# Optimization experiments

Hardware: AMD Instinct MI355X
Metric: run time of the kernel (lower is better)

The kernel has to match this reference:

```python
import jax, jax.numpy as jnp
import numpy as np

B = 64          # number of jets
LVLS = 13       # tree levels (complete binary tree, 4096 leaves/jet)
F = 7           # input features
H = 64          # hidden size
SIZES = [B * (2 ** j) for j in range(LVLS)]
OFFS = np.concatenate([[0], np.cumsum(SIZES)])  # level offsets into flat contents


def setup_inputs() -> dict:
    key = jax.random.key(0)
    ks = jax.random.split(key, 9)
    n_total = int(OFFS[-1])  # 524224
    s = lambda k, shp, fan: jax.random.normal(k, shp, jnp.float32) / np.sqrt(fan)
    return {
        "contents": jax.random.normal(ks[0], (n_total, F), jnp.float32),
        "W_u": s(ks[1], (H, F), F),       "b_u": jnp.zeros((H,), jnp.float32),
        "W_r": s(ks[2], (3 * H, 3 * H), 3 * H), "b_r": jnp.zeros((3 * H,), jnp.float32),
        "W_h": s(ks[3], (H, 3 * H), 3 * H),     "b_h": jnp.zeros((H,), jnp.float32),
        "W_z": s(ks[4], (4 * H, 4 * H), 4 * H), "b_z": jnp.zeros((4 * H,), jnp.float32),
    }


def reference(contents, W_u, b_u, W_r, b_r, W_h, b_h, W_z, b_z):
    # Bottom-up recursive gated embedding (n_iters=0 path -> relu activation).
    up = None  # embedding of level j+1
    for j in reversed(range(LVLS)):
        c = contents[int(OFFS[j]):int(OFFS[j + 1])]        # [n_j, F]
        u = jax.nn.relu(c @ W_u.T + b_u)                   # [n_j, H]
        if j == LVLS - 1:
            up = u                                         # leaf level: no inners
            continue
        n = SIZES[j]
        # children of node k are (2k, 2k+1) at level j+1 -> strided gather
        h_L = up[0::2]                                     # [n_j, H]
        h_R = up[1::2]                                     # [n_j, H]
        hhu = jnp.concatenate([h_L, h_R, u], axis=1)       # [n_j, 3H]
        r = jax.nn.sigmoid(hhu @ W_r.T + b_r)              # reset gate
        h_H = jax.nn.relu((r * hhu) @ W_h.T + b_h)         # candidate
        z = jnp.concatenate([h_H, hhu], axis=1) @ W_z.T + b_z  # [n_j, 4H]
        g = jax.nn.softmax(z.reshape(n, 4, H), axis=1)     # softmax over 4 gates
        up = g[:, 0] * h_H + g[:, 1] * h_L + g[:, 2] * h_R + g[:, 3] * u
    return up.reshape(B, -1)                               # [B, H]
```

## Files before the change

kernel.cpp:

```cpp
#include <hip/hip_runtime.h>
#include <hip/hip_bf16.h>


#define LOG2E 1.4426950408889634f
#define OSTR 76

typedef __bf16 bf16x8 __attribute__((ext_vector_type(8)));
typedef unsigned short u16x8 __attribute__((ext_vector_type(8)));
typedef float f32x4 __attribute__((ext_vector_type(4)));
typedef unsigned short bfr;

__device__ __forceinline__ float bfr2f(bfr v) { return __uint_as_float(((unsigned)v) << 16); }
__device__ __forceinline__ bfr f2bfr(float f) {
    __hip_bfloat16 h = __float2bfloat16(f);
    return __builtin_bit_cast(bfr, h);
}
__device__ __forceinline__ float fexp2(float x) {
#if __has_builtin(__builtin_amdgcn_exp2f)
    return __builtin_amdgcn_exp2f(x);
#else
    return exp2f(x);
#endif
}
__device__ __forceinline__ float frcp(float x) {
#if __has_builtin(__builtin_amdgcn_rcpf)
    return __builtin_amdgcn_rcpf(x);
#else
    return 1.f / x;
#endif
}

__device__ __forceinline__ int fidx(int Mt, int kt, int q, int ln, int KT) {
    return ((((Mt * KT + kt) * 4 + q) * 16 + ln) * 8);
}

__device__ __host__ __forceinline__ size_t lvloff(int j) {
    return (size_t)((64 << j) - 64) * 64;
}

__device__ __forceinline__ void pack_one(const float* __restrict__ W, bfr* __restrict__ dst,
                                         int d, int K, float scale) {
    int KT = K >> 5;
    int j = d & 7, lnc = (d >> 3) & 15, q = (d >> 7) & 3;
    int t1 = d >> 9;
    int kt = t1 % KT, ntile = t1 / KT;
    int ncol = ntile * 16 + lnc;
    int k = kt * 32 + q * 8 + j;
    dst[d] = f2bfr(W[(size_t)ncol * K + k] * scale);
}

__global__ void convert_weights(const float* __restrict__ Wr, const float* __restrict__ Wh,
                                const float* __restrict__ Wz, const float* __restrict__ Wu,
                                const float* __restrict__ br, const float* __restrict__ bz,
                                bfr* __restrict__ wr, bfr* __restrict__ wh, bfr* __restrict__ wz,
                                bfr* __restrict__ wu,
                                float* __restrict__ brs, float* __restrict__ bzs) {
    int i = blockIdx.x * 256 + threadIdx.x;
    if (i < 36864) pack_one(Wr, wr, i, 192, LOG2E);
    if (i < 12288) pack_one(Wh, wh, i, 192, 1.f);
    if (i < 65536) pack_one(Wz, wz, i, 256, LOG2E);
    if (i < 2048) {
        int j = i & 7, lnc = (i >> 3) & 15, q = (i >> 7) & 3, ntile = i >> 9;
        int k = q * 8 + j, ncol = ntile * 16 + lnc;
        wu[i] = (k < 7) ? f2bfr(Wu[ncol * 7 + k]) : (bfr)0;
    }
    if (i < 192) brs[i] = br[i] * LOG2E;
    if (i < 256) bzs[i] = bz[i] * LOG2E;
}

__device__ __forceinline__ void stage_c(const float* __restrict__ csrc, int rows,
                                        bfr* s_c) {
    const int tid = threadIdx.x;
    for (int t = tid; t < rows * 4; t += 256) {
        int row = t >> 2, qg = t & 3;
        ushort v[8] = {0, 0, 0, 0, 0, 0, 0, 0};
        if (qg == 0) {
            const float* cp = csrc + (size_t)row * 7;
#pragma unroll
            for (int k = 0; k < 7; ++k) v[k] = f2bfr(cp[k]);
        }
        *(uint4*)&s_c[(((row >> 4) * 4 + qg) * 16 + (row & 15)) * 8] = *(const uint4*)v;
    }
}

__device__ __forceinline__ bf16x8 load_c_frag(const float* __restrict__ c,
                                              size_t grow, bool active) {
    u16x8 cv = {0, 0, 0, 0, 0, 0, 0, 0};
    if (active) {
        const float* cp = c + grow * 7;
#pragma unroll
        for (int k = 0; k < 7; ++k) cv[k] = f2bfr(cp[k]);
    }
    return __builtin_bit_cast(bf16x8, cv);
}

__device__ __forceinline__ void store_up_coalesced(
    int row0, int rows, bfr* __restrict__ u_io,
    const ushort (&ovv)[4][4], int Mtn, bfr* s_t)
{
    const int tid = threadIdx.x;
    const int lane = tid & 63, w = tid >> 6;
    const int ln = lane & 15, q = lane >> 4;
    const int colbase = w * 16 + q * 4;
    __syncthreads();
#pragma unroll
    for (int Mt = 0; Mt < 4; ++Mt) {
        if (Mt < Mtn) {
            int row = Mt * 16 + ln;
            if (row < rows)
                *(uint2*)&s_t[row * OSTR + colbase] = *(const uint2*)ovv[Mt];
        }
    }
    __syncthreads();
#pragma unroll
    for (int it = 0; it < 2; ++it) {
        int idx = it * 256 + tid;
        int row = idx >> 3, ck = idx & 7;
        if (row < rows)
            *(uint4*)&u_io[(size_t)(row0 + row) * 64 + ck * 8] =
                *(const uint4*)&s_t[row * OSTR + ck * 8];
    }
}

template <bool CHILD_U>
__device__ __forceinline__ void tile_glob(
    int row0,
    const bfr* __restrict__ ch, const float* __restrict__ c_child,
    const float* __restrict__ c_own, bfr* __restrict__ u_io,
    const bfr* __restrict__ wu, const float* __restrict__ b_u,
    const bfr* __restrict__ wr, const float* __restrict__ brs,
    const bfr* __restrict__ wh, const float* __restrict__ b_h,
    const bfr* __restrict__ wz, const float* __restrict__ bzs,
    bfr* s_hhu, bfr* s_t)
{
    bfr* s_hH = s_t;
    const int tid = threadIdx.x;
    const int lane = tid & 63, w = tid >> 6;
    const int ln = lane & 15, q = lane >> 4;
    const int colbase = w * 16 + q * 4;

    float cof[4][7];
#pragma unroll
    for (int Mt = 0; Mt < 4; ++Mt) {
        const float* cp = c_own + (size_t)(row0 + Mt * 16 + ln) * 7;
#pragma unroll
        for (int k = 0; k < 7; ++k) cof[Mt][k] = (q == 0) ? cp[k] : 0.f;
    }
    bf16x8 awu = *(const bf16x8*)&wu[fidx(w, 0, q, ln, 1)];
    bf16x8 Af[3][6];
#pragma unroll
    for (int nt = 0; nt < 3; ++nt)
#pragma unroll
        for (int kt = 0; kt < 6; ++kt)
            Af[nt][kt] = *(const bf16x8*)&wr[fidx(w * 3 + nt, kt, q, ln, 6)];

    f32x4 bu4 = *(const f32x4*)&b_u[colbase];

    if (CHILD_U) {
        stage_c(c_child + (size_t)(2 * row0) * 7, 128, s_t + 2048);
        __syncthreads();
#pragma unroll
        for (int Mt = 0; Mt < 8; ++Mt) {
            bf16x8 Bc = *(const bf16x8*)&s_t[2048 + (((Mt * 4 + q) * 16 + ln) * 8)];
            f32x4 acc = {0.f, 0.f, 0.f, 0.f};
            acc = __builtin_amdgcn_mfma_f32_16x16x32_bf16(awu, Bc, acc, 0, 0, 0);
            int crow = Mt * 16 + ln;
            int row = crow >> 1;
            int kk = (crow & 1) * 64 + colbase;
            int addr = fidx(row >> 4, kk >> 5, (kk >> 3) & 3, row & 15, 6) + (kk & 7);
            ushort uv[4];
#pragma unroll
            for (int r = 0; r < 4; ++r) uv[r] = f2bfr(fmaxf(acc[r] + bu4[r], 0.f));
            *(uint2*)&s_hhu[addr] = *(const uint2*)uv;
        }
    } else {
#pragma unroll
        for (int it = 0; it < 4; ++it) {
            int idx = it * 256 + tid;
            int lns = idx & 15, qs = (idx >> 4) & 3, kts = (idx >> 6) & 3, Mts = idx >> 8;
            int row = Mts * 16 + lns;
            int k = kts * 32 + qs * 8;
            const bfr* src = (k < 64)
                ? ch + (size_t)(2 * (row0 + row)) * 64 + k
                : ch + (size_t)(2 * (row0 + row) + 1) * 64 + (k - 64);
            *(uint4*)&s_hhu[fidx(Mts, kts, qs, lns, 6)] = *(const uint4*)src;
        }
    }

#pragma unroll
    for (int Mt = 0; Mt < 4; ++Mt) {
        u16x8 cv = {0, 0, 0, 0, 0, 0, 0, 0};
        if (q == 0) {
#pragma unroll
            for (int k = 0; k < 7; ++k) cv[k] = f2bfr(cof[Mt][k]);
        }
        bf16x8 Bc = __builtin_bit_cast(bf16x8, cv);
        f32x4 acc = {0.f, 0.f, 0.f, 0.f};
        acc = __builtin_amdgcn_mfma_f32_16x16x32_bf16(awu, Bc, acc, 0, 0, 0);
        int kk = 128 + colbase;
        int addr = fidx(Mt, kk >> 5, (kk >> 3) & 3, ln, 6) + (kk & 7);
        ushort uv[4];
#pragma unroll
        for (int r = 0; r < 4; ++r) uv[r] = f2bfr(fmaxf(acc[r] + bu4[r], 0.f));
        *(uint2*)&s_hhu[addr] = *(const uint2*)uv;
    }
    __syncthreads();

    bf16x8 Ah[6];
#pragma unroll
    for (int kt = 0; kt < 6; ++kt)
        Ah[kt] = *(const bf16x8*)&wh[fidx(w, kt, q, ln, 6)];
    {
#pragma unroll
        for (int Mt = 0; Mt < 4; ++Mt) {
            bf16x8 Bf[6];
#pragma unroll
            for (int kt = 0; kt < 6; ++kt)
                Bf[kt] = *(const bf16x8*)&s_hhu[fidx(Mt, kt, q, ln, 6)];
#pragma unroll
            for (int nt = 0; nt < 3; ++nt) {
                int cb1 = (w * 3 + nt) * 16 + q * 4;
                f32x4 acc = {0.f, 0.f, 0.f, 0.f};
#pragma unroll
                for (int kt = 0; kt < 6; ++kt)
                    acc = __builtin_amdgcn_mfma_f32_16x16x32_bf16(Af[nt][kt], Bf[kt], acc, 0, 0, 0);
                f32x4 br4 = *(const f32x4*)&brs[cb1];
                int addr = fidx(Mt, cb1 >> 5, (cb1 >> 3) & 3, ln, 6) + (cb1 & 7);
                ushort hh[4], tt[4];
                *(uint2*)hh = *(const uint2*)&s_hhu[addr];
#pragma unroll
                for (int r = 0; r < 4; ++r) {
                    float e = fexp2(-(acc[r] + br4[r]));
                    tt[r] = f2bfr(frcp(1.f + e) * bfr2f(hh[r]));
                }
                *(uint2*)&s_t[addr] = *(const uint2*)tt;
            }
        }
    }
    __syncthreads();

    bf16x8 Awc[8], Awn[8];
#pragma unroll
    for (int kt = 0; kt < 8; ++kt)
        Awc[kt] = *(const bf16x8*)&wz[fidx(0 * 4 + w, kt, q, ln, 8)];
    f32x4 hacc[4];
    {
#pragma unroll
        for (int Mt = 0; Mt < 4; ++Mt) {
            f32x4 acc = {0.f, 0.f, 0.f, 0.f};
#pragma unroll
            for (int kt = 0; kt < 6; ++kt) {
                bf16x8 Bf = *(const bf16x8*)&s_t[fidx(Mt, kt, q, ln, 6)];
                acc = __builtin_amdgcn_mfma_f32_16x16x32_bf16(Ah[kt], Bf, acc, 0, 0, 0);
            }
            hacc[Mt] = acc;
        }
    }
    __syncthreads();
    {
        f32x4 bh4 = *(const f32x4*)&b_h[colbase];
#pragma unroll
        for (int Mt = 0; Mt < 4; ++Mt) {
            int addr = fidx(Mt, colbase >> 5, (colbase >> 3) & 3, ln, 2) + (colbase & 7);
            ushort hv[4];
#pragma unroll
            for (int r = 0; r < 4; ++r) hv[r] = f2bfr(fmaxf(hacc[Mt][r] + bh4[r], 0.f));
            *(uint2*)&s_hH[addr] = *(const uint2*)hv;
        }
    }
    __syncthreads();

    {
        f32x4 az[4][4];
#pragma unroll
        for (int g = 0; g < 4; ++g) {
            if (g < 3) {
#pragma unroll
                for (int kt = 0; kt < 8; ++kt)
                    Awn[kt] = *(const bf16x8*)&wz[fidx((g + 1) * 4 + w, kt, q, ln, 8)];
            }
#pragma unroll
            for (int Mt = 0; Mt < 4; ++Mt) {
                f32x4 acc = {0.f, 0.f, 0.f, 0.f};
                acc = __builtin_amdgcn_mfma_f32_16x16x32_bf16(
                    Awc[0], *(const bf16x8*)&s_hH[fidx(Mt, 0, q, ln, 2)], acc, 0, 0, 0);
                acc = __builtin_amdgcn_mfma_f32_16x16x32_bf16(
                    Awc[1], *(const bf16x8*)&s_hH[fidx(Mt, 1, q, ln, 2)], acc, 0, 0, 0);
#pragma unroll
                for (int kt = 0; kt < 6; ++kt)
                    acc = __builtin_amdgcn_mfma_f32_16x16x32_bf16(
                        Awc[2 + kt], *(const bf16x8*)&s_hhu[fidx(Mt, kt, q, ln, 6)], acc, 0, 0, 0);
                az[Mt][g] = acc;
            }
            if (g < 3) {
#pragma unroll
                for (int kt = 0; kt < 8; ++kt) Awc[kt] = Awn[kt];
            }
        }
        f32x4 bz0 = *(const f32x4*)&bzs[colbase];
        f32x4 bz1 = *(const f32x4*)&bzs[64 + colbase];
        f32x4 bz2 = *(const f32x4*)&bzs[128 + colbase];
        f32x4 bz3 = *(const f32x4*)&bzs[192 + colbase];
        ushort ovv[4][4];
#pragma unroll
        for (int Mt = 0; Mt < 4; ++Mt) {
            int aH = fidx(Mt, colbase >> 5, (colbase >> 3) & 3, ln, 2) + (colbase & 7);
            int a0 = fidx(Mt, colbase >> 5, (colbase >> 3) & 3, ln, 6) + (colbase & 7);
            int c1 = 64 + colbase, c2 = 128 + colbase;
            int a1 = fidx(Mt, c1 >> 5, (c1 >> 3) & 3, ln, 6) + (c1 & 7);
            int a2 = fidx(Mt, c2 >> 5, (c2 >> 3) & 3, ln, 6) + (c2 & 7);
            ushort hHv[4], u0[4], u1[4], u2[4];
            *(uint2*)hHv = *(const uint2*)&s_hH[aH];
            *(uint2*)u0 = *(const uint2*)&s_hhu[a0];
            *(uint2*)u1 = *(const uint2*)&s_hhu[a1];
            *(uint2*)u2 = *(const uint2*)&s_hhu[a2];
#pragma unroll
            for (int r = 0; r < 4; ++r) {
                float e0 = fexp2(az[Mt][0][r] + bz0[r]);
                float e1 = fexp2(az[Mt][1][r] + bz1[r]);
                float e2 = fexp2(az[Mt][2][r] + bz2[r]);
                float e3 = fexp2(az[Mt][3][r] + bz3[r]);
                float inv = frcp(e0 + e1 + e2 + e3);
                float v = (e0 * bfr2f(hHv[r]) + e1 * bfr2f(u0[r]) +
                           e2 * bfr2f(u1[r]) + e3 * bfr2f(u2[r])) * inv;
                ovv[Mt][r] = f2bfr(v);
            }
        }
        store_up_coalesced(row0, 64, u_io, ovv, 4, s_t);
    }
}

__global__ __launch_bounds__(256, 2) void level11_kernel(
    const float* __restrict__ c12, const float* __restrict__ c11,
    bfr* __restrict__ u_io,
    const bfr* __restrict__ wr, const float* __restrict__ brs,
    const bfr* __restrict__ wh, const float* __restrict__ b_h,
    const bfr* __restrict__ wz, const float* __restrict__ bzs,
    const bfr* __restrict__ wu, const float* __restrict__ b_u)
{
    __shared__ bfr s_hhu[12288];
    __shared__ bfr s_t[12288];
    tile_glob<true>(blockIdx.x * 64, nullptr, c12, c11, u_io,
                    wu, b_u, wr, brs, wh, b_h, wz, bzs, s_hhu, s_t);
}

__global__ __launch_bounds__(256, 2) void level_kernel(
    const bfr* __restrict__ ch, const float* __restrict__ c_own,
    bfr* __restrict__ u_io,
    const bfr* __restrict__ wr, const float* __restrict__ brs,
    const bfr* __restrict__ wh, const float* __restrict__ b_h,
    const bfr* __restrict__ wz, const float* __restrict__ bzs,
    const bfr* __restrict__ wu, const float* __restrict__ b_u)
{
    __shared__ bfr s_hhu[12288];
    __shared__ bfr s_t[12288];
    tile_glob<false>(blockIdx.x * 64, ch, nullptr, c_own, u_io,
                     wu, b_u, wr, brs, wh, b_h, wz, bzs, s_hhu, s_t);
}

__device__ __forceinline__ void load_wregs(
    const bfr* __restrict__ wr, const bfr* __restrict__ wh, const bfr* __restrict__ wz,
    const bfr* __restrict__ wu, int w, int q, int ln,
    bf16x8 (&Af)[3][6], bf16x8 (&Ah)[6], bf16x8 (&Aw)[4][8], bf16x8& awu)
{
#pragma unroll
    for (int nt = 0; nt < 3; ++nt)
#pragma unroll
        for (int kt = 0; kt < 6; ++kt)
            Af[nt][kt] = *(const bf16x8*)&wr[fidx(w * 3 + nt, kt, q, ln, 6)];
#pragma unroll
    for (int kt = 0; kt < 6; ++kt)
        Ah[kt] = *(const bf16x8*)&wh[fidx(w, kt, q, ln, 6)];
#pragma unroll
    for (int g = 0; g < 4; ++g)
#pragma unroll
        for (int kt = 0; kt < 8; ++kt)
            Aw[g][kt] = *(const bf16x8*)&wz[fidx(g * 4 + w, kt, q, ln, 8)];
    awu = *(const bf16x8*)&wu[fidx(w, 0, q, ln, 1)];
}

template <bool CH_LDS, bool STORE_U>
__device__ __forceinline__ void tile_regs(
    int row0, int rows,
    const bfr* __restrict__ ch, const float* __restrict__ c_own,
    bfr* __restrict__ u_io,
    const bf16x8 awu, const float* __restrict__ b_u,
    const bf16x8 (&Af)[3][6], const bf16x8 (&Ah)[6], const bf16x8 (&Aw)[4][8],
    const float* __restrict__ brs, const float* __restrict__ b_h,
    const float* __restrict__ bzs,
    float* __restrict__ outp, bfr* s_hhu, bfr* s_t, bfr* s_hH)
{
    const int tid = threadIdx.x;
    const int lane = tid & 63, w = tid >> 6;
    const int ln = lane & 15, q = lane >> 4;
    const int Mtn = (rows + 15) >> 4;
    const int colbase = w * 16 + q * 4;

    __syncthreads();

#pragma unroll
    for (int it = 0; it < 4; ++it) {
        int idx = it * 256 + tid;
        int lns = idx & 15, qs = (idx >> 4) & 3, kts = (idx >> 6) & 3, Mts = idx >> 8;
        int row = Mts * 16 + lns;
        if (row < rows) {
            int k = kts * 32 + qs * 8;
            if (CH_LDS) {
                int crow = 2 * row + (k >= 64 ? 1 : 0);
                *(uint4*)&s_hhu[fidx(Mts, kts, qs, lns, 6)] =
                    *(const uint4*)&s_t[crow * OSTR + (k & 63)];
            } else {
                const bfr* src = (k < 64)
                    ? ch + (size_t)(2 * (row0 + row)) * 64 + k
                    : ch + (size_t)(2 * (row0 + row) + 1) * 64 + (k - 64);
                *(uint4*)&s_hhu[fidx(Mts, kts, qs, lns, 6)] = *(const uint4*)src;
            }
        }
    }
    {
        f32x4 bu4 = *(const f32x4*)&b_u[colbase];
#pragma unroll
        for (int Mt = 0; Mt < 4; ++Mt) {
            if (Mt < Mtn) {
                int row = Mt * 16 + ln;
                bf16x8 Bc = load_c_frag(c_own, (size_t)row0 + row, q == 0 && row < rows);
                f32x4 acc = {0.f, 0.f, 0.f, 0.f};
                acc = __builtin_amdgcn_mfma_f32_16x16x32_bf16(awu, Bc, acc, 0, 0, 0);
                int kk = 128 + colbase;
                int addr = fidx(Mt, kk >> 5, (kk >> 3) & 3, ln, 6) + (kk & 7);
                ushort uv[4];
#pragma unroll
                for (int r = 0; r < 4; ++r) uv[r] = f2bfr(fmaxf(acc[r] + bu4[r], 0.f));
                *(uint2*)&s_hhu[addr] = *(const uint2*)uv;
            }
        }
    }
    __syncthreads();

#pragma unroll
    for (int Mt = 0; Mt < 4; ++Mt) {
        if (Mt < Mtn) {
            bf16x8 Bf[6];
#pragma unroll
            for (int kt = 0; kt < 6; ++kt)
                Bf[kt] = *(const bf16x8*)&s_hhu[fidx(Mt, kt, q, ln, 6)];
#pragma unroll
            for (int nt = 0; nt < 3; ++nt) {
                int cb1 = (w * 3 + nt) * 16 + q * 4;
                f32x4 acc = {0.f, 0.f, 0.f, 0.f};
#pragma unroll
                for (int kt = 0; kt < 6; ++kt)
                    acc = __builtin_amdgcn_mfma_f32_16x16x32_bf16(Af[nt][kt], Bf[kt], acc, 0, 0, 0);
                f32x4 br4 = *(const f32x4*)&brs[cb1];
                int addr = fidx(Mt, cb1 >> 5, (cb1 >> 3) & 3, ln, 6) + (cb1 & 7);
                ushort hh[4], tt[4];
                *(uint2*)hh = *(const uint2*)&s_hhu[addr];
#pragma unroll
                for (int r = 0; r < 4; ++r) {
                    float e = fexp2(-(acc[r] + br4[r]));
                    tt[r] = f2bfr(frcp(1.f + e) * bfr2f(hh[r]));
                }
                *(uint2*)&s_t[addr] = *(const uint2*)tt;
            }
        }
    }
    __syncthreads();

    {
        f32x4 bh4 = *(const f32x4*)&b_h[colbase];
#pragma unroll
        for (int Mt = 0; Mt < 4; ++Mt) {
            if (Mt < Mtn) {
                f32x4 acc = {0.f, 0.f, 0.f, 0.f};
#pragma unroll
                for (int kt = 0; kt < 6; ++kt) {
                    bf16x8 Bf = *(const bf16x8*)&s_t[fidx(Mt, kt, q, ln, 6)];
                    acc = __builtin_amdgcn_mfma_f32_16x16x32_bf16(Ah[kt], Bf, acc, 0, 0, 0);
                }
                int addr = fidx(Mt, colbase >> 5, (colbase >> 3) & 3, ln, 2) + (colbase & 7);
                ushort hv[4];
#pragma unroll
                for (int r = 0; r < 4; ++r) hv[r] = f2bfr(fmaxf(acc[r] + bh4[r], 0.f));
                *(uint2*)&s_hH[addr] = *(const uint2*)hv;
            }
        }
    }
    __syncthreads();

    {
        f32x4 bz0 = *(const f32x4*)&bzs[colbase];
        f32x4 bz1 = *(const f32x4*)&bzs[64 + colbase];
        f32x4 bz2 = *(const f32x4*)&bzs[128 + colbase];
        f32x4 bz3 = *(const f32x4*)&bzs[192 + colbase];
#pragma unroll
        for (int Mt = 0; Mt < 4; ++Mt) {
            if (Mt < Mtn) {
                bf16x8 Az[8];
                Az[0] = *(const bf16x8*)&s_hH[fidx(Mt, 0, q, ln, 2)];
                Az[1] = *(const bf16x8*)&s_hH[fidx(Mt, 1, q, ln, 2)];
#pragma unroll
                for (int kt = 0; kt < 6; ++kt)
                    Az[2 + kt] = *(const bf16x8*)&s_hhu[fidx(Mt, kt, q, ln, 6)];
                f32x4 azg[4];
#pragma unroll
                for (int g = 0; g < 4; ++g) {
                    f32x4 acc = {0.f, 0.f, 0.f, 0.f};
#pragma unroll
                    for (int kt = 0; kt < 8; ++kt)
                        acc = __builtin_amdgcn_mfma_f32_16x16x32_bf16(Aw[g][kt], Az[kt], acc, 0, 0, 0);
                    azg[g] = acc;
                }
                int row = Mt * 16 + ln;
                if (row < rows) {
                    int aH = fidx(Mt, colbase >> 5, (colbase >> 3) & 3, ln, 2) + (colbase & 7);
                    int a0 = fidx(Mt, colbase >> 5, (colbase >> 3) & 3, ln, 6) + (colbase & 7);
                    int c1 = 64 + colbase, c2 = 128 + colbase;
                    int a1 = fidx(Mt, c1 >> 5, (c1 >> 3) & 3, ln, 6) + (c1 & 7);
                    int a2 = fidx(Mt, c2 >> 5, (c2 >> 3) & 3, ln, 6) + (c2 & 7);
                    ushort hHv[4], u0[4], u1[4], u2[4], ov[4];
                    *(uint2*)hHv = *(const uint2*)&s_hH[aH];
                    *(uint2*)u0 = *(const uint2*)&s_hhu[a0];
                    *(uint2*)u1 = *(const uint2*)&s_hhu[a1];
                    *(uint2*)u2 = *(const uint2*)&s_hhu[a2];
                    float of[4];
#pragma unroll
                    for (int r = 0; r < 4; ++r) {
                        float e0 = fexp2(azg[0][r] + bz0[r]);
                        float e1 = fexp2(azg[1][r] + bz1[r]);
                        float e2 = fexp2(azg[2][r] + bz2[r]);
                        float e3 = fexp2(azg[3][r] + bz3[r]);
                        float inv = frcp(e0 + e1 + e2 + e3);
                        float v = (e0 * bfr2f(hHv[r]) + e1 * bfr2f(u0[r]) +
                                   e2 * bfr2f(u1[r]) + e3 * bfr2f(u2[r])) * inv;
                        ov[r] = f2bfr(v); of[r] = v;
                    }
                    *(uint2*)&s_t[row * OSTR + colbase] = *(const uint2*)ov;
                    if (outp)
                        *(float4*)&outp[(size_t)(row0 + row) * 64 + colbase] = *(const float4*)of;
                }
            }
        }
    }
    if (STORE_U) {
        __syncthreads();
        const int tid2 = threadIdx.x;
#pragma unroll
        for (int it = 0; it < 2; ++it) {
            int idx = it * 256 + tid2;
            int row = idx >> 3, ck = idx & 7;
            if (row < rows)
                *(uint4*)&u_io[(size_t)(row0 + row) * 64 + ck * 8] =
                    *(const uint4*)&s_t[row * OSTR + ck * 8];
        }
    }
}

__global__ __launch_bounds__(256, 1) void fused_mid_regs(
    const float* __restrict__ contents, bfr* __restrict__ u_all,
    const bfr* __restrict__ wr, const float* __restrict__ brs,
    const bfr* __restrict__ wh, const float* __restrict__ b_h,
    const bfr* __restrict__ wz, const float* __restrict__ bzs,
    const bfr* __restrict__ wu, const float* __restrict__ b_u)
{
    __shared__ bfr s_hhu[12288];
    __shared__ bfr s_t[12288];
    __shared__ bfr s_hH[4096];
    const int tid = threadIdx.x;
    const int lane = tid & 63, w = tid >> 6, ln = lane & 15, q = lane >> 4;
    bf16x8 Af[3][6], Ah[6], Aw[4][8], awu;
    load_wregs(wr, wh, wz, wu, w, q, ln, Af, Ah, Aw, awu);
    {
        const float* c8 = contents + (size_t)((64 << 8) - 64) * 7;
        tile_regs<false, false>(blockIdx.x * 64, 64,
                                u_all + lvloff(9), c8, u_all + lvloff(8),
                                awu, b_u, Af, Ah, Aw, brs, b_h, bzs,
                                nullptr, s_hhu, s_t, s_hH);
    }
    for (int j = 7; j >= 3; --j) {
        int rows = 1 << (j - 2);
        const float* c_own = contents + (size_t)((64 << j) - 64) * 7;
        tile_regs<true, false>(blockIdx.x * rows, rows,
                               nullptr, c_own, u_all + lvloff(j),
                               awu, b_u, Af, Ah, Aw, brs, b_h, bzs,
                               nullptr, s_hhu, s_t, s_hH);
    }
    {
        const float* c2 = contents + (size_t)((64 << 2) - 64) * 7;
        tile_regs<true, true>(blockIdx.x, 1,
                              nullptr, c2, u_all + lvloff(2),
                              awu, b_u, Af, Ah, Aw, brs, b_h, bzs,
                              nullptr, s_hhu, s_t, s_hH);
    }
}

__global__ __launch_bounds__(256, 1) void fused_tail_regs(
    const float* __restrict__ contents, bfr* __restrict__ u_all,
    const bfr* __restrict__ wr, const float* __restrict__ brs,
    const bfr* __restrict__ wh, const float* __restrict__ b_h,
    const bfr* __restrict__ wz, const float* __restrict__ bzs,
    const bfr* __restrict__ wu, const float* __restrict__ b_u,
    float* __restrict__ outp)
{
    __shared__ bfr s_hhu[12288];
    __shared__ bfr s_t[12288];
    __shared__ bfr s_hH[4096];
    const int tid = threadIdx.x;
    const int lane = tid & 63, w = tid >> 6, ln = lane & 15, q = lane >> 4;
    bf16x8 Af[3][6], Ah[6], Aw[4][8], awu;
    load_wregs(wr, wh, wz, wu, w, q, ln, Af, Ah, Aw, awu);
    {
        const float* c1 = contents + (size_t)((64 << 1) - 64) * 7;
        tile_regs<false, false>(blockIdx.x * 2, 2,
                                u_all + lvloff(2), c1, u_all + lvloff(1),
                                awu, b_u, Af, Ah, Aw, brs, b_h, bzs,
                                nullptr, s_hhu, s_t, s_hH);
    }
    {
        const float* c0 = contents;
        tile_regs<true, false>(blockIdx.x, 1,
                               nullptr, c0, u_all + lvloff(0),
                               awu, b_u, Af, Ah, Aw, brs, b_h, bzs,
                               outp, s_hhu, s_t, s_hH);
    }
}

extern "C" void kernel_launch(void* const* d_in, const int* in_sizes, int n_in,
                              void* d_out, int out_size, void* d_ws, size_t ws_size,
                              hipStream_t stream) {
    const float* contents = (const float*)d_in[0];
    const float* W_u = (const float*)d_in[1];
    const float* b_u = (const float*)d_in[2];
    const float* W_r = (const float*)d_in[3];
    const float* b_r = (const float*)d_in[4];
    const float* W_h = (const float*)d_in[5];
    const float* b_h = (const float*)d_in[6];
    const float* W_z = (const float*)d_in[7];
    const float* b_z = (const float*)d_in[8];
    float* out = (float*)d_out;

    bfr* u_all = (bfr*)d_ws;
    bfr* wr = u_all + (size_t)524224 * 64;
    bfr* wh = wr + 36864;
    bfr* wz = wh + 12288;
    float* brs = (float*)(wz + 65536);
    float* bzs = brs + 192;
    bfr* wu = (bfr*)(bzs + 256);

    convert_weights<<<256, 256, 0, stream>>>(W_r, W_h, W_z, W_u, b_r, b_z,
                                             wr, wh, wz, wu, brs, bzs);

    const float* c12 = contents + (size_t)((64 << 12) - 64) * 7;
    const float* c11 = contents + (size_t)((64 << 11) - 64) * 7;
    const float* c10 = contents + (size_t)((64 << 10) - 64) * 7;
    const float* c9  = contents + (size_t)((64 << 9) - 64) * 7;

    level11_kernel<<<2048, 256, 0, stream>>>(c12, c11, u_all + lvloff(11),
                                             wr, brs, wh, b_h, wz, bzs, wu, b_u);
    level_kernel<<<1024, 256, 0, stream>>>(u_all + lvloff(11), c10, u_all + lvloff(10),
                                           wr, brs, wh, b_h, wz, bzs, wu, b_u);
    level_kernel<<<512, 256, 0, stream>>>(u_all + lvloff(10), c9, u_all + lvloff(9),
                                          wr, brs, wh, b_h, wz, bzs, wu, b_u);
    fused_mid_regs<<<256, 256, 0, stream>>>(contents, u_all,
                                            wr, brs, wh, b_h, wz, bzs, wu, b_u);
    fused_tail_regs<<<64, 256, 0, stream>>>(contents, u_all,
                                            wr, brs, wh, b_h, wz, bzs, wu, b_u, out);
}
```

Baseline: 210.6 us.

## Fuse levels 11, 10 and 9 into one persistent kernel with register-resident weights

Replaces the three separate level kernels with a single kernel of 512 blocks, each of which processes four level-11 subtiles, two level-10 subtiles and one level-9 subtile in sequence. The W_h, W_z and W_u fragments are loaded into registers once per block and reused across all seven subtiles, and the own-node contents are staged through shared memory instead of per-thread loads. The W_z product is reordered so each row tile is consumed immediately rather than keeping all gate accumulators live. This removes two kernel launches and repeated weight loads, but it keeps many more registers live, drops the row-bound guard on the store, and lowers the grid size at the higher levels.

```diff
diff --git a/kernel.cpp b/kernel.cpp
--- a/kernel.cpp
+++ b/kernel.cpp
@@ -94,85 +94,45 @@
     return __builtin_bit_cast(bf16x8, cv);
 }
 
-__device__ __forceinline__ void store_up_coalesced(
-    int row0, int rows, bfr* __restrict__ u_io,
-    const ushort (&ovv)[4][4], int Mtn, bfr* s_t)
+__device__ __forceinline__ void mmu_own(const bfr* s_c, bfr* s_hhu, bf16x8 awu,
+                                        f32x4 bu4, int Mtn, int ln, int q,
+                                        int colbase) {
+#pragma unroll
+    for (int Mt = 0; Mt < 4; ++Mt) {
+        if (Mt < Mtn) {
+            bf16x8 Bc = *(const bf16x8*)&s_c[((Mt * 4 + q) * 16 + ln) * 8];
+            f32x4 acc = {0.f, 0.f, 0.f, 0.f};
+            acc = __builtin_amdgcn_mfma_f32_16x16x32_bf16(awu, Bc, acc, 0, 0, 0);
+            int kk = 128 + colbase;
+            int addr = fidx(Mt, kk >> 5, (kk >> 3) & 3, ln, 6) + (kk & 7);
+            ushort uv[4];
+#pragma unroll
+            for (int r = 0; r < 4; ++r) uv[r] = f2bfr(fmaxf(acc[r] + bu4[r], 0.f));
+            *(uint2*)&s_hhu[addr] = *(const uint2*)uv;
+        }
+    }
+}
+
+template <bool CHILD_U>
+__device__ __forceinline__ void subtile_top(
+    int row0,
+    const bfr* __restrict__ ch, const float* __restrict__ c_child,
+    const float* __restrict__ c_own, bfr* __restrict__ u_io,
+    const bf16x8 awu, const float* __restrict__ b_u,
+    const bfr* __restrict__ wr, const float* __restrict__ brs,
+    const bf16x8 (&Ah)[6], const float* __restrict__ b_h,
+    const bf16x8 (&Aw)[4][8], const float* __restrict__ bzs,
+    bfr* s_hhu, bfr* s_t, bfr* s_hH)
 {
     const int tid = threadIdx.x;
     const int lane = tid & 63, w = tid >> 6;
     const int ln = lane & 15, q = lane >> 4;
     const int colbase = w * 16 + q * 4;
-    __syncthreads();
-#pragma unroll
-    for (int Mt = 0; Mt < 4; ++Mt) {
-        if (Mt < Mtn) {
-            int row = Mt * 16 + ln;
-            if (row < rows)
-                *(uint2*)&s_t[row * OSTR + colbase] = *(const uint2*)ovv[Mt];
-        }
-    }
-    __syncthreads();
-#pragma unroll
-    for (int it = 0; it < 2; ++it) {
-        int idx = it * 256 + tid;
-        int row = idx >> 3, ck = idx & 7;
-        if (row < rows)
-            *(uint4*)&u_io[(size_t)(row0 + row) * 64 + ck * 8] =
-                *(const uint4*)&s_t[row * OSTR + ck * 8];
-    }
-}
-
-template <bool CHILD_U>
-__device__ __forceinline__ void tile_glob(
-    int row0,
-    const bfr* __restrict__ ch, const float* __restrict__ c_child,
-    const float* __restrict__ c_own, bfr* __restrict__ u_io,
-    const bfr* __restrict__ wu, const float* __restrict__ b_u,
-    const bfr* __restrict__ wr, const float* __restrict__ brs,
-    const bfr* __restrict__ wh, const float* __restrict__ b_h,
-    const bfr* __restrict__ wz, const float* __restrict__ bzs,
-    bfr* s_hhu, bfr* s_t)
-{
-    bfr* s_hH = s_t;
-    const int tid = threadIdx.x;
-    const int lane = tid & 63, w = tid >> 6;
-    const int ln = lane & 15, q = lane >> 4;
-    const int colbase = w * 16 + q * 4;
-
-    float cof[4][7];
-#pragma unroll
-    for (int Mt = 0; Mt < 4; ++Mt) {
-        const float* cp = c_own + (size_t)(row0 + Mt * 16 + ln) * 7;
-#pragma unroll
-        for (int k = 0; k < 7; ++k) cof[Mt][k] = (q == 0) ? cp[k] : 0.f;
-    }
-    bf16x8 awu = *(const bf16x8*)&wu[fidx(w, 0, q, ln, 1)];
-    bf16x8 Af[3][6];
-#pragma unroll
-    for (int nt = 0; nt < 3; ++nt)
-#pragma unroll
-        for (int kt = 0; kt < 6; ++kt)
-            Af[nt][kt] = *(const bf16x8*)&wr[fidx(w * 3 + nt, kt, q, ln, 6)];
-
-    f32x4 bu4 = *(const f32x4*)&b_u[colbase];
+
+    __syncthreads();
 
     if (CHILD_U) {
         stage_c(c_child + (size_t)(2 * row0) * 7, 128, s_t + 2048);
-        __syncthreads();
-#pragma unroll
-        for (int Mt = 0; Mt < 8; ++Mt) {
-            bf16x8 Bc = *(const bf16x8*)&s_t[2048 + (((Mt * 4 + q) * 16 + ln) * 8)];
-            f32x4 acc = {0.f, 0.f, 0.f, 0.f};
-            acc = __builtin_amdgcn_mfma_f32_16x16x32_bf16(awu, Bc, acc, 0, 0, 0);
-            int crow = Mt * 16 + ln;
-            int row = crow >> 1;
-            int kk = (crow & 1) * 64 + colbase;
-            int addr = fidx(row >> 4, kk >> 5, (kk >> 3) & 3, row & 15, 6) + (kk & 7);
-            ushort uv[4];
-#pragma unroll
-            for (int r = 0; r < 4; ++r) uv[r] = f2bfr(fmaxf(acc[r] + bu4[r], 0.f));
-            *(uint2*)&s_hhu[addr] = *(const uint2*)uv;
-        }
     } else {
 #pragma unroll
         for (int it = 0; it < 4; ++it) {
@@ -186,45 +146,52 @@
             *(uint4*)&s_hhu[fidx(Mts, kts, qs, lns, 6)] = *(const uint4*)src;
         }
     }
-
-#pragma unroll
-    for (int Mt = 0; Mt < 4; ++Mt) {
-        u16x8 cv = {0, 0, 0, 0, 0, 0, 0, 0};
-        if (q == 0) {
-#pragma unroll
-            for (int k = 0; k < 7; ++k) cv[k] = f2bfr(cof[Mt][k]);
-        }
-        bf16x8 Bc = __builtin_bit_cast(bf16x8, cv);
-        f32x4 acc = {0.f, 0.f, 0.f, 0.f};
-        acc = __builtin_amdgcn_mfma_f32_16x16x32_bf16(awu, Bc, acc, 0, 0, 0);
-        int kk = 128 + colbase;
-        int addr = fidx(Mt, kk >> 5, (kk >> 3) & 3, ln, 6) + (kk & 7);
-        ushort uv[4];
-#pragma unroll
-        for (int r = 0; r < 4; ++r) uv[r] = f2bfr(fmaxf(acc[r] + bu4[r], 0.f));
-        *(uint2*)&s_hhu[addr] = *(const uint2*)uv;
-    }
-    __syncthreads();
-
-    bf16x8 Ah[6];
-#pragma unroll
-    for (int kt = 0; kt < 6; ++kt)
-        Ah[kt] = *(const bf16x8*)&wh[fidx(w, kt, q, ln, 6)];
-    {
-#pragma unroll
-        for (int Mt = 0; Mt < 4; ++Mt) {
-            bf16x8 Bf[6];
-#pragma unroll
-            for (int kt = 0; kt < 6; ++kt)
-                Bf[kt] = *(const bf16x8*)&s_hhu[fidx(Mt, kt, q, ln, 6)];
-#pragma unroll
-            for (int nt = 0; nt < 3; ++nt) {
-                int cb1 = (w * 3 + nt) * 16 + q * 4;
+    stage_c(c_own + (size_t)row0 * 7, 64, s_t);
+    __syncthreads();
+
+    {
+        f32x4 bu4 = *(const f32x4*)&b_u[colbase];
+        if (CHILD_U) {
+#pragma unroll
+            for (int Mt = 0; Mt < 8; ++Mt) {
+                bf16x8 Bc = *(const bf16x8*)&s_t[2048 + (((Mt * 4 + q) * 16 + ln) * 8)];
                 f32x4 acc = {0.f, 0.f, 0.f, 0.f};
+                acc = __builtin_amdgcn_mfma_f32_16x16x32_bf16(awu, Bc, acc, 0, 0, 0);
+                int crow = Mt * 16 + ln;
+                int row = crow >> 1;
+                int kk = (crow & 1) * 64 + colbase;
+                int addr = fidx(row >> 4, kk >> 5, (kk >> 3) & 3, row & 15, 6) + (kk & 7);
+                ushort uv[4];
+#pragma unroll
+                for (int r = 0; r < 4; ++r) uv[r] = f2bfr(fmaxf(acc[r] + bu4[r], 0.f));
+                *(uint2*)&s_hhu[addr] = *(const uint2*)uv;
+            }
+        }
+        mmu_own(s_t, s_hhu, awu, bu4, 4, ln, q, colbase);
+    }
+    __syncthreads();
+
+    {
+        bf16x8 Afc[6], Afn[6];
+#pragma unroll
+        for (int kt = 0; kt < 6; ++kt)
+            Afc[kt] = *(const bf16x8*)&wr[fidx(w * 3, kt, q, ln, 6)];
+#pragma unroll
+        for (int nt = 0; nt < 3; ++nt) {
+            if (nt < 2) {
 #pragma unroll
                 for (int kt = 0; kt < 6; ++kt)
-                    acc = __builtin_amdgcn_mfma_f32_16x16x32_bf16(Af[nt][kt], Bf[kt], acc, 0, 0, 0);
-                f32x4 br4 = *(const f32x4*)&brs[cb1];
+                    Afn[kt] = *(const bf16x8*)&wr[fidx(w * 3 + nt + 1, kt, q, ln, 6)];
+            }
+            int cb1 = (w * 3 + nt) * 16 + q * 4;
+            f32x4 br4 = *(const f32x4*)&brs[cb1];
+#pragma unroll
+            for (int Mt = 0; Mt < 4; ++Mt) {
+                f32x4 acc = {0.f, 0.f, 0.f, 0.f};
+#pragma unroll
+                for (int kt = 0; kt < 6; ++kt)
+                    acc = __builtin_amdgcn_mfma_f32_16x16x32_bf16(
+                        Afc[kt], *(const bf16x8*)&s_hhu[fidx(Mt, kt, q, ln, 6)], acc, 0, 0, 0);
                 int addr = fidx(Mt, cb1 >> 5, (cb1 >> 3) & 3, ln, 6) + (cb1 & 7);
                 ushort hh[4], tt[4];
                 *(uint2*)hh = *(const uint2*)&s_hhu[addr];
@@ -235,104 +202,92 @@
                 }
                 *(uint2*)&s_t[addr] = *(const uint2*)tt;
             }
-        }
-    }
-    __syncthreads();
-
-    bf16x8 Awc[8], Awn[8];
-#pragma unroll
-    for (int kt = 0; kt < 8; ++kt)
-        Awc[kt] = *(const bf16x8*)&wz[fidx(0 * 4 + w, kt, q, ln, 8)];
-    f32x4 hacc[4];
-    {
+            if (nt < 2) {
+#pragma unroll
+                for (int kt = 0; kt < 6; ++kt) Afc[kt] = Afn[kt];
+            }
+        }
+    }
+    __syncthreads();
+
+    {
+        f32x4 bh4 = *(const f32x4*)&b_h[colbase];
 #pragma unroll
         for (int Mt = 0; Mt < 4; ++Mt) {
             f32x4 acc = {0.f, 0.f, 0.f, 0.f};
 #pragma unroll
-            for (int kt = 0; kt < 6; ++kt) {
-                bf16x8 Bf = *(const bf16x8*)&s_t[fidx(Mt, kt, q, ln, 6)];
-                acc = __builtin_amdgcn_mfma_f32_16x16x32_bf16(Ah[kt], Bf, acc, 0, 0, 0);
-            }
-            hacc[Mt] = acc;
-        }
-    }
-    __syncthreads();
-    {
-        f32x4 bh4 = *(const f32x4*)&b_h[colbase];
-#pragma unroll
-        for (int Mt = 0; Mt < 4; ++Mt) {
+            for (int kt = 0; kt < 6; ++kt)
+                acc = __builtin_amdgcn_mfma_f32_16x16x32_bf16(
+                    Ah[kt], *(const bf16x8*)&s_t[fidx(Mt, kt, q, ln, 6)], acc, 0, 0, 0);
             int addr = fidx(Mt, colbase >> 5, (colbase >> 3) & 3, ln, 2) + (colbase & 7);
             ushort hv[4];
 #pragma unroll
-            for (int r = 0; r < 4; ++r) hv[r] = f2bfr(fmaxf(hacc[Mt][r] + bh4[r], 0.f));
+            for (int r = 0; r < 4; ++r) hv[r] = f2bfr(fmaxf(acc[r] + bh4[r], 0.f));
             *(uint2*)&s_hH[addr] = *(const uint2*)hv;
         }
     }
     __syncthreads();
 
     {
-        f32x4 az[4][4];
-#pragma unroll
-        for (int g = 0; g < 4; ++g) {
-            if (g < 3) {
-#pragma unroll
-                for (int kt = 0; kt < 8; ++kt)
-                    Awn[kt] = *(const bf16x8*)&wz[fidx((g + 1) * 4 + w, kt, q, ln, 8)];
-            }
-#pragma unroll
-            for (int Mt = 0; Mt < 4; ++Mt) {
-                f32x4 acc = {0.f, 0.f, 0.f, 0.f};
-                acc = __builtin_amdgcn_mfma_f32_16x16x32_bf16(
-                    Awc[0], *(const bf16x8*)&s_hH[fidx(Mt, 0, q, ln, 2)], acc, 0, 0, 0);
-                acc = __builtin_amdgcn_mfma_f32_16x16x32_bf16(
-                    Awc[1], *(const bf16x8*)&s_hH[fidx(Mt, 1, q, ln, 2)], acc, 0, 0, 0);
-#pragma unroll
-                for (int kt = 0; kt < 6; ++kt)
-                    acc = __builtin_amdgcn_mfma_f32_16x16x32_bf16(
-                        Awc[2 + kt], *(const bf16x8*)&s_hhu[fidx(Mt, kt, q, ln, 6)], acc, 0, 0, 0);
-                az[Mt][g] = acc;
-            }
-            if (g < 3) {
-#pragma unroll
-                for (int kt = 0; kt < 8; ++kt) Awc[kt] = Awn[kt];
-            }
-        }
         f32x4 bz0 = *(const f32x4*)&bzs[colbase];
         f32x4 bz1 = *(const f32x4*)&bzs[64 + colbase];
         f32x4 bz2 = *(const f32x4*)&bzs[128 + colbase];
         f32x4 bz3 = *(const f32x4*)&bzs[192 + colbase];
-        ushort ovv[4][4];
 #pragma unroll
         for (int Mt = 0; Mt < 4; ++Mt) {
+            bf16x8 Az[8];
+            Az[0] = *(const bf16x8*)&s_hH[fidx(Mt, 0, q, ln, 2)];
+            Az[1] = *(const bf16x8*)&s_hH[fidx(Mt, 1, q, ln, 2)];
+#pragma unroll
+            for (int kt = 0; kt < 6; ++kt)
+                Az[2 + kt] = *(const bf16x8*)&s_hhu[fidx(Mt, kt, q, ln, 6)];
+            f32x4 azg[4];
+#pragma unroll
+            for (int g = 0; g < 4; ++g) {
+                f32x4 acc = {0.f, 0.f, 0.f, 0.f};
+#pragma unroll
+                for (int kt = 0; kt < 8; ++kt)
+                    acc = __builtin_amdgcn_mfma_f32_16x16x32_bf16(Aw[g][kt], Az[kt], acc, 0, 0, 0);
+                azg[g] = acc;
+            }
+            int row = Mt * 16 + ln;
             int aH = fidx(Mt, colbase >> 5, (colbase >> 3) & 3, ln, 2) + (colbase & 7);
             int a0 = fidx(Mt, colbase >> 5, (colbase >> 3) & 3, ln, 6) + (colbase & 7);
             int c1 = 64 + colbase, c2 = 128 + colbase;
             int a1 = fidx(Mt, c1 >> 5, (c1 >> 3) & 3, ln, 6) + (c1 & 7);
             int a2 = fidx(Mt, c2 >> 5, (c2 >> 3) & 3, ln, 6) + (c2 & 7);
-            ushort hHv[4], u0[4], u1[4], u2[4];
+            ushort hHv[4], u0[4], u1[4], u2[4], ov[4];
             *(uint2*)hHv = *(const uint2*)&s_hH[aH];
             *(uint2*)u0 = *(const uint2*)&s_hhu[a0];
             *(uint2*)u1 = *(const uint2*)&s_hhu[a1];
             *(uint2*)u2 = *(const uint2*)&s_hhu[a2];
 #pragma unroll
             for (int r = 0; r < 4; ++r) {
-                float e0 = fexp2(az[Mt][0][r] + bz0[r]);
-                float e1 = fexp2(az[Mt][1][r] + bz1[r]);
-                float e2 = fexp2(az[Mt][2][r] + bz2[r]);
-                float e3 = fexp2(az[Mt][3][r] + bz3[r]);
+                float e0 = fexp2(azg[0][r] + bz0[r]);
+                float e1 = fexp2(azg[1][r] + bz1[r]);
+                float e2 = fexp2(azg[2][r] + bz2[r]);
+                float e3 = fexp2(azg[3][r] + bz3[r]);
                 float inv = frcp(e0 + e1 + e2 + e3);
                 float v = (e0 * bfr2f(hHv[r]) + e1 * bfr2f(u0[r]) +
                            e2 * bfr2f(u1[r]) + e3 * bfr2f(u2[r])) * inv;
-                ovv[Mt][r] = f2bfr(v);
-            }
-        }
-        store_up_coalesced(row0, 64, u_io, ovv, 4, s_t);
-    }
-}
-
-__global__ __launch_bounds__(256, 2) void level11_kernel(
-    const float* __restrict__ c12, const float* __restrict__ c11,
-    bfr* __restrict__ u_io,
+                ov[r] = f2bfr(v);
+            }
+            *(uint2*)&s_t[row * OSTR + colbase] = *(const uint2*)ov;
+        }
+    }
+    __syncthreads();
+
+#pragma unroll
+    for (int it = 0; it < 2; ++it) {
+        int idx = it * 256 + tid;
+        int row = idx >> 3, ck = idx & 7;
+        *(uint4*)&u_io[(size_t)(row0 + row) * 64 + ck * 8] =
+            *(const uint4*)&s_t[row * OSTR + ck * 8];
+    }
+}
+
+__global__ __launch_bounds__(256, 2) void levels_top_kernel(
+    const float* __restrict__ contents, bfr* __restrict__ u_all,
     const bfr* __restrict__ wr, const float* __restrict__ brs,
     const bfr* __restrict__ wh, const float* __restrict__ b_h,
     const bfr* __restrict__ wz, const float* __restrict__ bzs,
@@ -340,22 +295,39 @@
 {
     __shared__ bfr s_hhu[12288];
     __shared__ bfr s_t[12288];
-    tile_glob<true>(blockIdx.x * 64, nullptr, c12, c11, u_io,
-                    wu, b_u, wr, brs, wh, b_h, wz, bzs, s_hhu, s_t);
-}
-
-__global__ __launch_bounds__(256, 2) void level_kernel(
-    const bfr* __restrict__ ch, const float* __restrict__ c_own,
-    bfr* __restrict__ u_io,
-    const bfr* __restrict__ wr, const float* __restrict__ brs,
-    const bfr* __restrict__ wh, const float* __restrict__ b_h,
-    const bfr* __restrict__ wz, const float* __restrict__ bzs,
-    const bfr* __restrict__ wu, const float* __restrict__ b_u)
-{
-    __shared__ bfr s_hhu[12288];
-    __shared__ bfr s_t[12288];
-    tile_glob<false>(blockIdx.x * 64, ch, nullptr, c_own, u_io,
-                     wu, b_u, wr, brs, wh, b_h, wz, bzs, s_hhu, s_t);
+    __shared__ bfr s_hH[4096];
+    const int tid = threadIdx.x;
+    const int lane = tid & 63, w = tid >> 6, ln = lane & 15, q = lane >> 4;
+
+    bf16x8 Ah[6], Aw[4][8], awu;
+#pragma unroll
+    for (int kt = 0; kt < 6; ++kt)
+        Ah[kt] = *(const bf16x8*)&wh[fidx(w, kt, q, ln, 6)];
+#pragma unroll
+    for (int g = 0; g < 4; ++g)
+#pragma unroll
+        for (int kt = 0; kt < 8; ++kt)
+            Aw[g][kt] = *(const bf16x8*)&wz[fidx(g * 4 + w, kt, q, ln, 8)];
+    awu = *(const bf16x8*)&wu[fidx(w, 0, q, ln, 1)];
+
+    const float* c12 = contents + (size_t)((64 << 12) - 64) * 7;
+    const float* c11 = contents + (size_t)((64 << 11) - 64) * 7;
+    const float* c10 = contents + (size_t)((64 << 10) - 64) * 7;
+    const float* c9  = contents + (size_t)((64 << 9)  - 64) * 7;
+    bfr* u11 = u_all + lvloff(11);
+    bfr* u10 = u_all + lvloff(10);
+    bfr* u9  = u_all + lvloff(9);
+
+#pragma unroll 1
+    for (int t = 0; t < 4; ++t)
+        subtile_top<true>(blockIdx.x * 256 + t * 64, nullptr, c12, c11, u11,
+                          awu, b_u, wr, brs, Ah, b_h, Aw, bzs, s_hhu, s_t, s_hH);
+#pragma unroll 1
+    for (int t = 0; t < 2; ++t)
+        subtile_top<false>(blockIdx.x * 128 + t * 64, u11, nullptr, c10, u10,
+                           awu, b_u, wr, brs, Ah, b_h, Aw, bzs, s_hhu, s_t, s_hH);
+    subtile_top<false>(blockIdx.x * 64, u10, nullptr, c9, u9,
+                       awu, b_u, wr, brs, Ah, b_h, Aw, bzs, s_hhu, s_t, s_hH);
 }
 
 __device__ __forceinline__ void load_wregs(
@@ -649,17 +621,8 @@
     convert_weights<<<256, 256, 0, stream>>>(W_r, W_h, W_z, W_u, b_r, b_z,
                                              wr, wh, wz, wu, brs, bzs);
 
-    const float* c12 = contents + (size_t)((64 << 12) - 64) * 7;
-    const float* c11 = contents + (size_t)((64 << 11) - 64) * 7;
-    const float* c10 = contents + (size_t)((64 << 10) - 64) * 7;
-    const float* c9  = contents + (size_t)((64 << 9) - 64) * 7;
-
-    level11_kernel<<<2048, 256, 0, stream>>>(c12, c11, u_all + lvloff(11),
-                                             wr, brs, wh, b_h, wz, bzs, wu, b_u);
-    level_kernel<<<1024, 256, 0, stream>>>(u_all + lvloff(11), c10, u_all + lvloff(10),
-                                           wr, brs, wh, b_h, wz, bzs, wu, b_u);
-    level_kernel<<<512, 256, 0, stream>>>(u_all + lvloff(10), c9, u_all + lvloff(9),
-                                          wr, brs, wh, b_h, wz, bzs, wu, b_u);
+    levels_top_kernel<<<512, 256, 0, stream>>>(contents, u_all,
+                                               wr, brs, wh, b_h, wz, bzs, wu, b_u);
     fused_mid_regs<<<256, 256, 0, stream>>>(contents, u_all,
                                             wr, brs, wh, b_h, wz, bzs, wu, b_u);
     fused_tail_regs<<<64, 256, 0, stream>>>(contents, u_all,
```

Result: slower. 426.0 us (+102.3%).

## Fuse levels 11, 10 and 9 into one subtree kernel with per-block tiling

Applied to the files above, without the earlier changes.

Replaces the three separate kernel launches for levels 11, 10 and 9 with a single kernel. Each block processes four 64-row tiles of level 11, then the two level-10 tiles and the one level-9 tile whose children it just wrote. This removes two launches and their inter-kernel gaps, and keeps the intermediate embeddings in cache for reuse. Weight register loads are moved into narrower scopes, and own-level contents are now staged through LDS, to lower register pressure. The trade-off is only 512 blocks and serialized tiles per block. The fused design also relies on the block's own global writes to u11 and u10 being visible to its later reads after __syncthreads.

```diff
diff --git a/kernel.cpp b/kernel.cpp
--- a/kernel.cpp
+++ b/kernel.cpp
@@ -122,8 +122,27 @@
     }
 }
 
+__device__ __forceinline__ void mmu_own(const bfr* s_c, bfr* s_hhu, bf16x8 awu,
+                                        f32x4 bu4, int Mtn, int ln, int q,
+                                        int colbase) {
+#pragma unroll
+    for (int Mt = 0; Mt < 4; ++Mt) {
+        if (Mt < Mtn) {
+            bf16x8 Bc = *(const bf16x8*)&s_c[((Mt * 4 + q) * 16 + ln) * 8];
+            f32x4 acc = {0.f, 0.f, 0.f, 0.f};
+            acc = __builtin_amdgcn_mfma_f32_16x16x32_bf16(awu, Bc, acc, 0, 0, 0);
+            int kk = 128 + colbase;
+            int addr = fidx(Mt, kk >> 5, (kk >> 3) & 3, ln, 6) + (kk & 7);
+            ushort uv[4];
+#pragma unroll
+            for (int r = 0; r < 4; ++r) uv[r] = f2bfr(fmaxf(acc[r] + bu4[r], 0.f));
+            *(uint2*)&s_hhu[addr] = *(const uint2*)uv;
+        }
+    }
+}
+
 template <bool CHILD_U>
-__device__ __forceinline__ void tile_glob(
+__device__ __forceinline__ void subtile_top(
     int row0,
     const bfr* __restrict__ ch, const float* __restrict__ c_child,
     const float* __restrict__ c_own, bfr* __restrict__ u_io,
@@ -139,41 +158,9 @@
     const int ln = lane & 15, q = lane >> 4;
     const int colbase = w * 16 + q * 4;
 
-    float cof[4][7];
-#pragma unroll
-    for (int Mt = 0; Mt < 4; ++Mt) {
-        const float* cp = c_own + (size_t)(row0 + Mt * 16 + ln) * 7;
-#pragma unroll
-        for (int k = 0; k < 7; ++k) cof[Mt][k] = (q == 0) ? cp[k] : 0.f;
-    }
-    bf16x8 awu = *(const bf16x8*)&wu[fidx(w, 0, q, ln, 1)];
-    bf16x8 Af[3][6];
-#pragma unroll
-    for (int nt = 0; nt < 3; ++nt)
-#pragma unroll
-        for (int kt = 0; kt < 6; ++kt)
-            Af[nt][kt] = *(const bf16x8*)&wr[fidx(w * 3 + nt, kt, q, ln, 6)];
-
-    f32x4 bu4 = *(const f32x4*)&b_u[colbase];
-
-    if (CHILD_U) {
-        stage_c(c_child + (size_t)(2 * row0) * 7, 128, s_t + 2048);
-        __syncthreads();
-#pragma unroll
-        for (int Mt = 0; Mt < 8; ++Mt) {
-            bf16x8 Bc = *(const bf16x8*)&s_t[2048 + (((Mt * 4 + q) * 16 + ln) * 8)];
-            f32x4 acc = {0.f, 0.f, 0.f, 0.f};
-            acc = __builtin_amdgcn_mfma_f32_16x16x32_bf16(awu, Bc, acc, 0, 0, 0);
-            int crow = Mt * 16 + ln;
-            int row = crow >> 1;
-            int kk = (crow & 1) * 64 + colbase;
-            int addr = fidx(row >> 4, kk >> 5, (kk >> 3) & 3, row & 15, 6) + (kk & 7);
-            ushort uv[4];
-#pragma unroll
-            for (int r = 0; r < 4; ++r) uv[r] = f2bfr(fmaxf(acc[r] + bu4[r], 0.f));
-            *(uint2*)&s_hhu[addr] = *(const uint2*)uv;
-        }
-    } else {
+    __syncthreads();
+
+    if (!CHILD_U) {
 #pragma unroll
         for (int it = 0; it < 4; ++it) {
             int idx = it * 256 + tid;
@@ -185,32 +172,42 @@
                 : ch + (size_t)(2 * (row0 + row) + 1) * 64 + (k - 64);
             *(uint4*)&s_hhu[fidx(Mts, kts, qs, lns, 6)] = *(const uint4*)src;
         }
-    }
-
-#pragma unroll
-    for (int Mt = 0; Mt < 4; ++Mt) {
-        u16x8 cv = {0, 0, 0, 0, 0, 0, 0, 0};
-        if (q == 0) {
-#pragma unroll
-            for (int k = 0; k < 7; ++k) cv[k] = f2bfr(cof[Mt][k]);
-        }
-        bf16x8 Bc = __builtin_bit_cast(bf16x8, cv);
-        f32x4 acc = {0.f, 0.f, 0.f, 0.f};
-        acc = __builtin_amdgcn_mfma_f32_16x16x32_bf16(awu, Bc, acc, 0, 0, 0);
-        int kk = 128 + colbase;
-        int addr = fidx(Mt, kk >> 5, (kk >> 3) & 3, ln, 6) + (kk & 7);
-        ushort uv[4];
-#pragma unroll
-        for (int r = 0; r < 4; ++r) uv[r] = f2bfr(fmaxf(acc[r] + bu4[r], 0.f));
-        *(uint2*)&s_hhu[addr] = *(const uint2*)uv;
-    }
-    __syncthreads();
-
-    bf16x8 Ah[6];
-#pragma unroll
-    for (int kt = 0; kt < 6; ++kt)
-        Ah[kt] = *(const bf16x8*)&wh[fidx(w, kt, q, ln, 6)];
-    {
+    } else {
+        stage_c(c_child + (size_t)(2 * row0) * 7, 128, s_t + 2048);
+    }
+    stage_c(c_own + (size_t)row0 * 7, 64, s_t);
+    __syncthreads();
+
+    {
+        bf16x8 awu = *(const bf16x8*)&wu[fidx(w, 0, q, ln, 1)];
+        f32x4 bu4 = *(const f32x4*)&b_u[colbase];
+        if (CHILD_U) {
+#pragma unroll
+            for (int Mt = 0; Mt < 8; ++Mt) {
+                bf16x8 Bc = *(const bf16x8*)&s_t[2048 + (((Mt * 4 + q) * 16 + ln) * 8)];
+                f32x4 acc = {0.f, 0.f, 0.f, 0.f};
+                acc = __builtin_amdgcn_mfma_f32_16x16x32_bf16(awu, Bc, acc, 0, 0, 0);
+                int crow = Mt * 16 + ln;
+                int row = crow >> 1;
+                int kk = (crow & 1) * 64 + colbase;
+                int addr = fidx(row >> 4, kk >> 5, (kk >> 3) & 3, row & 15, 6) + (kk & 7);
+                ushort uv[4];
+#pragma unroll
+                for (int r = 0; r < 4; ++r) uv[r] = f2bfr(fmaxf(acc[r] + bu4[r], 0.f));
+                *(uint2*)&s_hhu[addr] = *(const uint2*)uv;
+            }
+        }
+        mmu_own(s_t, s_hhu, awu, bu4, 4, ln, q, colbase);
+    }
+    __syncthreads();
+
+    {
+        bf16x8 Af[3][6];
+#pragma unroll
+        for (int nt = 0; nt < 3; ++nt)
+#pragma unroll
+            for (int kt = 0; kt < 6; ++kt)
+                Af[nt][kt] = *(const bf16x8*)&wr[fidx(w * 3 + nt, kt, q, ln, 6)];
 #pragma unroll
         for (int Mt = 0; Mt < 4; ++Mt) {
             bf16x8 Bf[6];
@@ -239,12 +236,12 @@
     }
     __syncthreads();
 
-    bf16x8 Awc[8], Awn[8];
-#pragma unroll
-    for (int kt = 0; kt < 8; ++kt)
-        Awc[kt] = *(const bf16x8*)&wz[fidx(0 * 4 + w, kt, q, ln, 8)];
     f32x4 hacc[4];
     {
+        bf16x8 Ah[6];
+#pragma unroll
+        for (int kt = 0; kt < 6; ++kt)
+            Ah[kt] = *(const bf16x8*)&wh[fidx(w, kt, q, ln, 6)];
 #pragma unroll
         for (int Mt = 0; Mt < 4; ++Mt) {
             f32x4 acc = {0.f, 0.f, 0.f, 0.f};
@@ -273,28 +270,27 @@
     {
         f32x4 az[4][4];
 #pragma unroll
+        for (int Mt = 0; Mt < 4; ++Mt)
+#pragma unroll
+            for (int g = 0; g < 4; ++g) az[Mt][g] = (f32x4){0.f, 0.f, 0.f, 0.f};
+#pragma unroll
         for (int g = 0; g < 4; ++g) {
-            if (g < 3) {
-#pragma unroll
-                for (int kt = 0; kt < 8; ++kt)
-                    Awn[kt] = *(const bf16x8*)&wz[fidx((g + 1) * 4 + w, kt, q, ln, 8)];
-            }
+            bf16x8 Aw[8];
+#pragma unroll
+            for (int kt = 0; kt < 8; ++kt)
+                Aw[kt] = *(const bf16x8*)&wz[fidx(g * 4 + w, kt, q, ln, 8)];
 #pragma unroll
             for (int Mt = 0; Mt < 4; ++Mt) {
-                f32x4 acc = {0.f, 0.f, 0.f, 0.f};
+                f32x4 acc = az[Mt][g];
                 acc = __builtin_amdgcn_mfma_f32_16x16x32_bf16(
-                    Awc[0], *(const bf16x8*)&s_hH[fidx(Mt, 0, q, ln, 2)], acc, 0, 0, 0);
+                    Aw[0], *(const bf16x8*)&s_hH[fidx(Mt, 0, q, ln, 2)], acc, 0, 0, 0);
                 acc = __builtin_amdgcn_mfma_f32_16x16x32_bf16(
-                    Awc[1], *(const bf16x8*)&s_hH[fidx(Mt, 1, q, ln, 2)], acc, 0, 0, 0);
+                    Aw[1], *(const bf16x8*)&s_hH[fidx(Mt, 1, q, ln, 2)], acc, 0, 0, 0);
 #pragma unroll
                 for (int kt = 0; kt < 6; ++kt)
                     acc = __builtin_amdgcn_mfma_f32_16x16x32_bf16(
-                        Awc[2 + kt], *(const bf16x8*)&s_hhu[fidx(Mt, kt, q, ln, 6)], acc, 0, 0, 0);
+                        Aw[2 + kt], *(const bf16x8*)&s_hhu[fidx(Mt, kt, q, ln, 6)], acc, 0, 0, 0);
                 az[Mt][g] = acc;
-            }
-            if (g < 3) {
-#pragma unroll
-                for (int kt = 0; kt < 8; ++kt) Awc[kt] = Awn[kt];
             }
         }
         f32x4 bz0 = *(const f32x4*)&bzs[colbase];
@@ -330,9 +326,8 @@
     }
 }
 
-__global__ __launch_bounds__(256, 2) void level11_kernel(
-    const float* __restrict__ c12, const float* __restrict__ c11,
-    bfr* __restrict__ u_io,
+__global__ __launch_bounds__(256, 2) void levels_top_kernel(
+    const float* __restrict__ contents, bfr* __restrict__ u_all,
     const bfr* __restrict__ wr, const float* __restrict__ brs,
     const bfr* __restrict__ wh, const float* __restrict__ b_h,
     const bfr* __restrict__ wz, const float* __restrict__ bzs,
@@ -340,22 +335,25 @@
 {
     __shared__ bfr s_hhu[12288];
     __shared__ bfr s_t[12288];
-    tile_glob<true>(blockIdx.x * 64, nullptr, c12, c11, u_io,
-                    wu, b_u, wr, brs, wh, b_h, wz, bzs, s_hhu, s_t);
-}
-
-__global__ __launch_bounds__(256, 2) void level_kernel(
-    const bfr* __restrict__ ch, const float* __restrict__ c_own,
-    bfr* __restrict__ u_io,
-    const bfr* __restrict__ wr, const float* __restrict__ brs,
-    const bfr* __restrict__ wh, const float* __restrict__ b_h,
-    const bfr* __restrict__ wz, const float* __restrict__ bzs,
-    const bfr* __restrict__ wu, const float* __restrict__ b_u)
-{
-    __shared__ bfr s_hhu[12288];
-    __shared__ bfr s_t[12288];
-    tile_glob<false>(blockIdx.x * 64, ch, nullptr, c_own, u_io,
-                     wu, b_u, wr, brs, wh, b_h, wz, bzs, s_hhu, s_t);
+
+    const float* c12 = contents + (size_t)((64 << 12) - 64) * 7;
+    const float* c11 = contents + (size_t)((64 << 11) - 64) * 7;
+    const float* c10 = contents + (size_t)((64 << 10) - 64) * 7;
+    const float* c9  = contents + (size_t)((64 << 9)  - 64) * 7;
+    bfr* u11 = u_all + lvloff(11);
+    bfr* u10 = u_all + lvloff(10);
+    bfr* u9  = u_all + lvloff(9);
+
+#pragma unroll 1
+    for (int t = 0; t < 4; ++t)
+        subtile_top<true>(blockIdx.x * 256 + t * 64, nullptr, c12, c11, u11,
+                          wu, b_u, wr, brs, wh, b_h, wz, bzs, s_hhu, s_t);
+#pragma unroll 1
+    for (int t = 0; t < 2; ++t)
+        subtile_top<false>(blockIdx.x * 128 + t * 64, u11, nullptr, c10, u10,
+                           wu, b_u, wr, brs, wh, b_h, wz, bzs, s_hhu, s_t);
+    subtile_top<false>(blockIdx.x * 64, u10, nullptr, c9, u9,
+                       wu, b_u, wr, brs, wh, b_h, wz, bzs, s_hhu, s_t);
 }
 
 __device__ __forceinline__ void load_wregs(
@@ -649,17 +647,8 @@
     convert_weights<<<256, 256, 0, stream>>>(W_r, W_h, W_z, W_u, b_r, b_z,
                                              wr, wh, wz, wu, brs, bzs);
 
-    const float* c12 = contents + (size_t)((64 << 12) - 64) * 7;
-    const float* c11 = contents + (size_t)((64 << 11) - 64) * 7;
-    const float* c10 = contents + (size_t)((64 << 10) - 64) * 7;
-    const float* c9  = contents + (size_t)((64 << 9) - 64) * 7;
-
-    level11_kernel<<<2048, 256, 0, stream>>>(c12, c11, u_all + lvloff(11),
-                                             wr, brs, wh, b_h, wz, bzs, wu, b_u);
-    level_kernel<<<1024, 256, 0, stream>>>(u_all + lvloff(11), c10, u_all + lvloff(10),
-                                           wr, brs, wh, b_h, wz, bzs, wu, b_u);
-    level_kernel<<<512, 256, 0, stream>>>(u_all + lvloff(10), c9, u_all + lvloff(9),
-                                          wr, brs, wh, b_h, wz, bzs, wu, b_u);
+    levels_top_kernel<<<512, 256, 0, stream>>>(contents, u_all,
+                                               wr, brs, wh, b_h, wz, bzs, wu, b_u);
     fused_mid_regs<<<256, 256, 0, stream>>>(contents, u_all,
                                             wr, brs, wh, b_h, wz, bzs, wu, b_u);
     fused_tail_regs<<<64, 256, 0, stream>>>(contents, u_all,
```

After: 406.9 us. 93.2% more time.
